# Performance work log

Hardware: AMD Instinct MI355X
Metric: run time of the kernel (lower is better)

## Reference

```python
import jax, jax.numpy as jnp
import numpy as np

D_MODEL = 1024
N_HEADS = 16
HEAD_DIM = D_MODEL // N_HEADS
ROPE_BASE = 10000.0


def setup_inputs() -> dict:
    key = jax.random.key(0)
    ks = jax.random.split(key, 5)
    B, S = 4, 2048
    bound_qkv = 1.0 / np.sqrt(D_MODEL)
    bound_out = 1.0 / np.sqrt(D_MODEL)
    return {
        "query": jax.random.normal(ks[0], (B, S, D_MODEL), dtype=jnp.float32),
        "W_qkv": jax.random.uniform(ks[1], (3 * D_MODEL, D_MODEL), jnp.float32, -bound_qkv, bound_qkv),
        "b_qkv": jax.random.uniform(ks[2], (3 * D_MODEL,), jnp.float32, -bound_qkv, bound_qkv),
        "W_out": jax.random.uniform(ks[3], (D_MODEL, D_MODEL), jnp.float32, -bound_out, bound_out),
        "b_out": jax.random.uniform(ks[4], (D_MODEL,), jnp.float32, -bound_out, bound_out),
    }


def _rope(x):
    # x: [B, H, S, Dh]; rotate-half RoPE, full rotational fraction
    S, Dh = x.shape[2], x.shape[3]
    half = Dh // 2
    inv_freq = 1.0 / (ROPE_BASE ** (jnp.arange(0, half, dtype=jnp.float32) * 2.0 / Dh))
    ang = jnp.arange(S, dtype=jnp.float32)[:, None] * inv_freq[None, :]  # [S, half]
    cos = jnp.concatenate([jnp.cos(ang), jnp.cos(ang)], axis=-1)  # [S, Dh]
    sin = jnp.concatenate([jnp.sin(ang), jnp.sin(ang)], axis=-1)
    x1, x2 = x[..., :half], x[..., half:]
    rot = jnp.concatenate([-x2, x1], axis=-1)
    return x * cos + rot * sin


def reference(query, W_qkv, b_qkv, W_out, b_out):
    B, S, _ = query.shape
    qkv = query @ W_qkv.T + b_qkv  # [B, S, 3*D]
    qkv = qkv.reshape(B, S, 3, N_HEADS, HEAD_DIM).transpose(2, 0, 3, 1, 4)  # [3, B, H, S, Dh]
    q, k, v = qkv[0], qkv[1], qkv[2]
    q = _rope(q)
    k = _rope(k)
    scale = 1.0 / np.sqrt(HEAD_DIM)
    scores = jnp.einsum("bhsd,bhtd->bhst", q, k) * scale  # [B, H, S, S]
    attn = jax.nn.softmax(scores, axis=-1)
    out = jnp.einsum("bhst,bhtd->bhsd", attn, v)  # [B, H, S, Dh]
    out = out.transpose(0, 2, 1, 3).reshape(B, S, D_MODEL)
    return out @ W_out.T + b_out
```

## Files before the change

kernel.cpp:

```cpp
#include <hip/hip_runtime.h>
#include <math.h>

#define D_MODEL 1024
#define N_HEADS 16
#define HEAD_DIM 64
#define BATCH 4
#define SEQ 2048
#define TOKENS (BATCH * SEQ)

typedef _Float16 f16;
typedef f16 f16x8_t __attribute__((ext_vector_type(8)));
typedef f16 f16x4_t __attribute__((ext_vector_type(4)));
typedef float f32x4_t __attribute__((ext_vector_type(4)));

#define QSCALE 0.18033688011112042f

#define KSW(row, g) ((g) ^ ((row) & 7))

__device__ __forceinline__ void stage16(const f16* g, f16* l) {
    __builtin_amdgcn_global_load_lds(
        (__attribute__((address_space(1))) void*)g,
        (__attribute__((address_space(3))) void*)l, 16, 0, 0);
}

#define N_X  (TOKENS * D_MODEL / 4)
#define N_WQ (3 * D_MODEL * D_MODEL / 4)
#define N_WO (D_MODEL * D_MODEL / 4)
#define N_CONV (N_X + N_WQ + N_WO)
__global__ void prep_kernel(const float* __restrict__ X,
                            const float* __restrict__ Wq,
                            const float* __restrict__ Wo,
                            f16* __restrict__ Xf, f16* __restrict__ Wqf,
                            f16* __restrict__ Wof,
                            float* __restrict__ cosT, float* __restrict__ sinT) {
    int i = blockIdx.x * blockDim.x + threadIdx.x;
    if (i >= N_CONV) {
        int idx = i - N_CONV;
        int s = idx >> 5;
        int ii = idx & 31;
        double t = (double)(2 * ii) / 64.0;
        double invf = pow(10000.0, -t);
        double ang = (double)s * invf;
        cosT[idx] = (float)cos(ang);
        sinT[idx] = (float)sin(ang);
        return;
    }
    const float* src;
    f16* dst;
    int j;
    if (i < N_X)             { src = X;  dst = Xf;  j = i; }
    else if (i < N_X + N_WQ) { src = Wq; dst = Wqf; j = i - N_X; }
    else                     { src = Wo; dst = Wof; j = i - N_X - N_WQ; }
    float4 x = ((const float4*)src)[j];
    f16x4_t h;
    h[0] = (f16)x.x; h[1] = (f16)x.y; h[2] = (f16)x.z; h[3] = (f16)x.w;
    ((f16x4_t*)dst)[j] = h;
}

__device__ __forceinline__ void gemm_mainloop(
    const f16* __restrict__ A, const f16* __restrict__ B,
    int n0, int c0, f16* As, f16* Bs, f32x4_t acc[4][4]) {
    const int tid = threadIdx.x;
    const int lane = tid & 63;
    const int wave = tid >> 6;
    const int m16 = lane & 15, quad = lane >> 4;
    const int wm = (wave & 1) * 64, wn = (wave >> 1) * 64;

    const int srow  = lane >> 3;
    const int sgran = (lane & 7) ^ srow;

#pragma unroll
    for (int i = 0; i < 4; i++)
#pragma unroll
        for (int j = 0; j < 4; j++) acc[i][j] = (f32x4_t){0.f, 0.f, 0.f, 0.f};

    f16* ldsA = As + (wave * 32) * 64;
    f16* ldsB = Bs + (wave * 32) * 64;
    const f16* ga = A + (size_t)(n0 + wave * 32 + srow) * D_MODEL + sgran * 8;
    const f16* gb = B + (size_t)(c0 + wave * 32 + srow) * D_MODEL + sgran * 8;

    for (int kt = 0; kt < 16; kt++) {
        const int ko = kt * 64;
        __syncthreads();
#pragma unroll
        for (int inst = 0; inst < 4; inst++) {
            stage16(ga + ko + (size_t)(inst * 8) * D_MODEL, ldsA + inst * 8 * 64);
            stage16(gb + ko + (size_t)(inst * 8) * D_MODEL, ldsB + inst * 8 * 64);
        }
        __syncthreads();
#pragma unroll
        for (int kk = 0; kk < 2; kk++) {
            f16x8_t a[4], b[4];
#pragma unroll
            for (int mt = 0; mt < 4; mt++) {
                const int row = wm + mt * 16 + m16;
                a[mt] = *(const f16x8_t*)&As[row * 64 + KSW(row, kk * 4 + quad) * 8];
            }
#pragma unroll
            for (int nt = 0; nt < 4; nt++) {
                const int row = wn + nt * 16 + m16;
                b[nt] = *(const f16x8_t*)&Bs[row * 64 + KSW(row, kk * 4 + quad) * 8];
            }
#pragma unroll
            for (int mt = 0; mt < 4; mt++)
#pragma unroll
                for (int nt = 0; nt < 4; nt++)
                    acc[mt][nt] = __builtin_amdgcn_mfma_f32_16x16x32_f16(
                        a[mt], b[nt], acc[mt][nt], 0, 0, 0);
        }
    }
}

__global__ __launch_bounds__(256)
void qkv_gemm_kernel(const f16* __restrict__ Xf, const f16* __restrict__ Wf,
                     const float* __restrict__ bias,
                     f16* __restrict__ Qb, f16* __restrict__ Kb,
                     f16* __restrict__ VbT,
                     const float* __restrict__ cosT, const float* __restrict__ sinT) {
    __shared__ f16 As[128 * 64];
    __shared__ f16 Bs[128 * 64];
    f32x4_t acc[4][4];
    const int n0 = blockIdx.y * 128;
    const int c0 = blockIdx.x * 128;
    gemm_mainloop(Xf, Wf, n0, c0, As, Bs, acc);

    const int lane = threadIdx.x & 63;
    const int wave = threadIdx.x >> 6;
    const int m16 = lane & 15, quad = lane >> 4;
    const int wm = (wave & 1) * 64, wn = (wave >> 1) * 64;

    const int w = c0 >> 10;
    const int hh = ((c0 + wn) & 1023) >> 6;
    const int b = n0 >> 11;

    float bias4[4];
#pragma unroll
    for (int nt = 0; nt < 4; nt++) bias4[nt] = bias[c0 + wn + nt * 16 + m16];

    if (w == 2) {
        f16* vbase = VbT + ((size_t)(b * N_HEADS + hh) * HEAD_DIM) * SEQ;
#pragma unroll
        for (int mt = 0; mt < 4; mt++) {
            const int sbl = (n0 + wm + (mt >> 1) * 32) & (SEQ - 1);
            const int sb  = sbl + quad * 8 + (mt & 1) * 4;
#pragma unroll
            for (int nt = 0; nt < 4; nt++) {
                const int dh = nt * 16 + m16;
                f16x4_t v4;
#pragma unroll
                for (int i = 0; i < 4; i++) v4[i] = (f16)(acc[mt][nt][i] + bias4[nt]);
                *(f16x4_t*)&vbase[(size_t)dh * SEQ + sb] = v4;
            }
        }
        return;
    }

    f16* dst = (w == 0) ? Qb : Kb;
#pragma unroll
    for (int mt = 0; mt < 4; mt++)
#pragma unroll
        for (int i = 0; i < 4; i++) {
            const int n = n0 + wm + mt * 16 + quad * 4 + i;
            const int s = n & (SEQ - 1);
            f16* drow = dst + ((size_t)(b * N_HEADS + hh) * SEQ + s) * HEAD_DIM;
            float vv[4];
#pragma unroll
            for (int nt = 0; nt < 4; nt++) vv[nt] = acc[mt][nt][i] + bias4[nt];
            const float cs0 = cosT[(s << 5) + m16];
            const float sn0 = sinT[(s << 5) + m16];
            const float cs1 = cosT[(s << 5) + 16 + m16];
            const float sn1 = sinT[(s << 5) + 16 + m16];
#pragma unroll
            for (int nt = 0; nt < 4; nt++) {
                const int dh = nt * 16 + m16;
                const float cs = (nt & 1) ? cs1 : cs0;
                const float sn = (nt & 1) ? sn1 : sn0;
                const float part = vv[nt ^ 2];
                float outv = (nt >= 2) ? fmaf(vv[nt], cs, part * sn)
                                       : fmaf(vv[nt], cs, -part * sn);
                if (w == 0) outv *= QSCALE;
                drow[dh] = (f16)outv;
            }
        }
}

__global__ __launch_bounds__(256)
void out_gemm_kernel(const f16* __restrict__ Of, const f16* __restrict__ Wf,
                     const float* __restrict__ bias, float* __restrict__ Cout) {
    __shared__ f16 As[128 * 64];
    __shared__ f16 Bs[128 * 64];
    f32x4_t acc[4][4];
    const int n0 = blockIdx.y * 128;
    const int c0 = blockIdx.x * 128;
    gemm_mainloop(Of, Wf, n0, c0, As, Bs, acc);

    const int lane = threadIdx.x & 63;
    const int wave = threadIdx.x >> 6;
    const int m16 = lane & 15, quad = lane >> 4;
    const int wm = (wave & 1) * 64, wn = (wave >> 1) * 64;

    float bias4[4];
#pragma unroll
    for (int nt = 0; nt < 4; nt++) bias4[nt] = bias[c0 + wn + nt * 16 + m16];

#pragma unroll
    for (int mt = 0; mt < 4; mt++)
#pragma unroll
        for (int i = 0; i < 4; i++) {
            const int n = n0 + wm + mt * 16 + quad * 4 + i;
            float* orow = Cout + (size_t)n * D_MODEL + c0 + wn;
#pragma unroll
            for (int nt = 0; nt < 4; nt++)
                orow[nt * 16 + m16] = acc[mt][nt][i] + bias4[nt];
        }
}

#define NT (SEQ / 64)
__global__ __launch_bounds__(256, 2)
void attn_kernel(const f16* __restrict__ Qb, const f16* __restrict__ Kb,
                 const f16* __restrict__ VbT, f16* __restrict__ Of) {
    __shared__ f16 Ks[2][64 * 64];
    __shared__ f16 Vs[2][64 * 64];

    const int tid  = threadIdx.x;
    const int lane = tid & 63;
    const int wave = tid >> 6;
    const int m16  = lane & 15;
    const int quad = lane >> 4;

    const int bh = blockIdx.x & 63;
    const int qt = blockIdx.x >> 6;
    const int s0 = qt * 256;

    const f16* Kbase  = Kb + (size_t)bh * SEQ * HEAD_DIM;
    const f16* VtBase = VbT + (size_t)bh * HEAD_DIM * SEQ;

    f16x8_t bq[4][2];
#pragma unroll
    for (int nq = 0; nq < 4; nq++) {
        const f16* qrow = Qb + ((size_t)bh * SEQ + s0 + wave * 64 + nq * 16 + m16)
                          * HEAD_DIM + quad * 8;
        bq[nq][0] = *(const f16x8_t*)(qrow);
        bq[nq][1] = *(const f16x8_t*)(qrow + 32);
    }

    f32x4_t Oc[4][4];
#pragma unroll
    for (int mt = 0; mt < 4; mt++)
#pragma unroll
        for (int nq = 0; nq < 4; nq++) Oc[mt][nq] = (f32x4_t){0.f, 0.f, 0.f, 0.f};
    float sumacc[4] = {0.f, 0.f, 0.f, 0.f};

    const int lrow0 = wave * 16 + (lane >> 3);
    const int lrow1 = lrow0 + 8;
    const int gK0 = lrow0 * HEAD_DIM + KSW(lrow0, lane & 7) * 8;
    const int gK1 = lrow1 * HEAD_DIM + KSW(lrow1, lane & 7) * 8;
    const int gV0 = lrow0 * SEQ + KSW(lrow0, lane & 7) * 8;
    const int gV1 = lrow1 * SEQ + KSW(lrow1, lane & 7) * 8;
    const int lO0 = (wave * 16) * 64;
    const int lO1 = (wave * 16 + 8) * 64;

    stage16(Kbase + gK0, &Ks[0][lO0]);
    stage16(Kbase + gK1, &Ks[0][lO1]);
    stage16(VtBase + gV0, &Vs[0][lO0]);
    stage16(VtBase + gV1, &Vs[0][lO1]);
    asm volatile("s_waitcnt vmcnt(0)" ::: "memory");
    __builtin_amdgcn_s_barrier();
    asm volatile("" ::: "memory");

    for (int kt = 0; kt < NT; kt++) {
        const int cur = kt & 1;

        if (kt + 1 < NT) {
            const f16* kg = Kbase + (size_t)(kt + 1) * 64 * HEAD_DIM;
            const f16* vg = VtBase + (kt + 1) * 64;
            f16* kd = &Ks[cur ^ 1][0];
            f16* vd = &Vs[cur ^ 1][0];
            stage16(kg + gK0, kd + lO0);
            stage16(kg + gK1, kd + lO1);
            stage16(vg + gV0, vd + lO0);
            stage16(vg + gV1, vd + lO1);
        }

        const f16* Kc = &Ks[cur][0];
        const f16* Vc = &Vs[cur][0];

        f32x4_t Sc[4][4];
#pragma unroll
        for (int nt = 0; nt < 4; nt++)
#pragma unroll
            for (int nq = 0; nq < 4; nq++) Sc[nt][nq] = (f32x4_t){0.f, 0.f, 0.f, 0.f};
#pragma unroll
        for (int kki = 0; kki < 2; kki++) {
#pragma unroll
            for (int nt = 0; nt < 4; nt++) {
                const int row = nt * 16 + m16;
                f16x8_t ak = *(const f16x8_t*)&Kc[row * 64 + KSW(row, kki * 4 + quad) * 8];
                __builtin_amdgcn_s_setprio(1);
#pragma unroll
                for (int nq = 0; nq < 4; nq++)
                    Sc[nt][nq] = __builtin_amdgcn_mfma_f32_16x16x32_f16(
                        ak, bq[nq][kki], Sc[nt][nq], 0, 0, 0);
                __builtin_amdgcn_s_setprio(0);
            }
        }

#pragma unroll
        for (int kki = 0; kki < 2; kki++) {
            f16x8_t bp[4];
#pragma unroll
            for (int nq = 0; nq < 4; nq++)
#pragma unroll
                for (int h = 0; h < 2; h++) {
                    const int nt = 2 * kki + h;
#pragma unroll
                    for (int i = 0; i < 4; i++) {
                        float p = __builtin_amdgcn_exp2f(Sc[nt][nq][i]);
                        sumacc[nq] += p;
                        bp[nq][h * 4 + i] = (f16)p;
                    }
                }
#pragma unroll
            for (int mt = 0; mt < 4; mt++) {
                const int d = mt * 16 + m16;
                f16x8_t av = *(const f16x8_t*)&Vc[d * 64 + KSW(d, kki * 4 + quad) * 8];
                __builtin_amdgcn_s_setprio(1);
#pragma unroll
                for (int nq = 0; nq < 4; nq++)
                    Oc[mt][nq] = __builtin_amdgcn_mfma_f32_16x16x32_f16(
                        av, bp[nq], Oc[mt][nq], 0, 0, 0);
                __builtin_amdgcn_s_setprio(0);
            }
        }

        asm volatile("s_waitcnt vmcnt(0)" ::: "memory");
        __builtin_amdgcn_s_barrier();
        asm volatile("" ::: "memory");
    }

    const int b = bh >> 4, h = bh & 15;
#pragma unroll
    for (int nq = 0; nq < 4; nq++) {
        float l = sumacc[nq];
        l += __shfl_xor(l, 16);
        l += __shfl_xor(l, 32);
        const float invl = 1.0f / l;
        const int s = s0 + wave * 64 + nq * 16 + m16;
        const size_t off = ((size_t)(b * SEQ + s)) * D_MODEL + h * HEAD_DIM;
#pragma unroll
        for (int mt = 0; mt < 4; mt++) {
            f16x4_t o4;
#pragma unroll
            for (int i = 0; i < 4; i++)
                o4[i] = (f16)(Oc[mt][nq][i] * invl);
            *(f16x4_t*)&Of[off + mt * 16 + quad * 4] = o4;
        }
    }
}

extern "C" void kernel_launch(void* const* d_in, const int* in_sizes, int n_in,
                              void* d_out, int out_size, void* d_ws, size_t ws_size,
                              hipStream_t stream) {
    const float* X    = (const float*)d_in[0];
    const float* Wqkv = (const float*)d_in[1];
    const float* bqkv = (const float*)d_in[2];
    const float* Wout = (const float*)d_in[3];
    const float* bout = (const float*)d_in[4];
    float* out = (float*)d_out;

    char* w8 = (char*)d_ws;
    const size_t MB = 1024 * 1024;
    f16* Xf  = (f16*)(w8);
    f16* Wqf = (f16*)(w8 + 16 * MB);
    f16* Wof = (f16*)(w8 + 22 * MB);
    f16* Qf  = (f16*)(w8 + 24 * MB);
    f16* Kf  = (f16*)(w8 + 40 * MB);
    f16* VfT = (f16*)(w8 + 56 * MB);
    f16* Of  = (f16*)(w8 + 72 * MB);
    float* cosT = (float*)(w8 + 88 * MB);
    float* sinT = cosT + SEQ * 32;

    prep_kernel<<<(N_CONV + SEQ * 32) / 256, 256, 0, stream>>>(
        X, Wqkv, Wout, Xf, Wqf, Wof, cosT, sinT);

    qkv_gemm_kernel<<<dim3(3 * D_MODEL / 128, TOKENS / 128), 256, 0, stream>>>(
        Xf, Wqf, bqkv, Qf, Kf, VfT, cosT, sinT);
    attn_kernel<<<64 * (SEQ / 256), 256, 0, stream>>>(Qf, Kf, VfT, Of);
    out_gemm_kernel<<<dim3(D_MODEL / 128, TOKENS / 128), 256, 0, stream>>>(
        Of, Wof, bout, out);
}
```

Before: 270.5 us.

## Double-buffer GEMM mainloop LDS staging with BK=32 and prefetch next tile

```diff
diff --git a/kernel.cpp b/kernel.cpp
--- a/kernel.cpp
+++ b/kernel.cpp
@@ -16,6 +16,7 @@
 #define QSCALE 0.18033688011112042f
 
 #define KSW(row, g) ((g) ^ ((row) & 7))
+#define GSW(row, g) ((g) ^ (((row) >> 1) & 3))
 
 __device__ __forceinline__ void stage16(const f16* g, f16* l) {
     __builtin_amdgcn_global_load_lds(
@@ -57,6 +58,10 @@
     ((f16x4_t*)dst)[j] = h;
 }
 
+#define GBK 32
+#define GNKT (D_MODEL / GBK)
+#define GBUF (128 * GBK)
+
 __device__ __forceinline__ void gemm_mainloop(
     const f16* __restrict__ A, const f16* __restrict__ B,
     int n0, int c0, f16* As, f16* Bs, f32x4_t acc[4][4]) {
@@ -66,48 +71,64 @@
     const int m16 = lane & 15, quad = lane >> 4;
     const int wm = (wave & 1) * 64, wn = (wave >> 1) * 64;
 
-    const int srow  = lane >> 3;
-    const int sgran = (lane & 7) ^ srow;
+    const int srow = lane >> 2;
+    const int sg   = (lane & 3) ^ ((lane >> 3) & 3);
 
 #pragma unroll
     for (int i = 0; i < 4; i++)
 #pragma unroll
         for (int j = 0; j < 4; j++) acc[i][j] = (f32x4_t){0.f, 0.f, 0.f, 0.f};
 
-    f16* ldsA = As + (wave * 32) * 64;
-    f16* ldsB = Bs + (wave * 32) * 64;
-    const f16* ga = A + (size_t)(n0 + wave * 32 + srow) * D_MODEL + sgran * 8;
-    const f16* gb = B + (size_t)(c0 + wave * 32 + srow) * D_MODEL + sgran * 8;
-
-    for (int kt = 0; kt < 16; kt++) {
-        const int ko = kt * 64;
-        __syncthreads();
-#pragma unroll
-        for (int inst = 0; inst < 4; inst++) {
-            stage16(ga + ko + (size_t)(inst * 8) * D_MODEL, ldsA + inst * 8 * 64);
-            stage16(gb + ko + (size_t)(inst * 8) * D_MODEL, ldsB + inst * 8 * 64);
-        }
-        __syncthreads();
-#pragma unroll
-        for (int kk = 0; kk < 2; kk++) {
-            f16x8_t a[4], b[4];
-#pragma unroll
-            for (int mt = 0; mt < 4; mt++) {
-                const int row = wm + mt * 16 + m16;
-                a[mt] = *(const f16x8_t*)&As[row * 64 + KSW(row, kk * 4 + quad) * 8];
-            }
-#pragma unroll
-            for (int nt = 0; nt < 4; nt++) {
-                const int row = wn + nt * 16 + m16;
-                b[nt] = *(const f16x8_t*)&Bs[row * 64 + KSW(row, kk * 4 + quad) * 8];
-            }
-#pragma unroll
-            for (int mt = 0; mt < 4; mt++)
-#pragma unroll
-                for (int nt = 0; nt < 4; nt++)
-                    acc[mt][nt] = __builtin_amdgcn_mfma_f32_16x16x32_f16(
-                        a[mt], b[nt], acc[mt][nt], 0, 0, 0);
-        }
+    const f16* ga = A + (size_t)(n0 + wave * 32 + srow) * D_MODEL + sg * 8;
+    const f16* gb = B + (size_t)(c0 + wave * 32 + srow) * D_MODEL + sg * 8;
+    f16* la = As + (wave * 32) * GBK;
+    f16* lb = Bs + (wave * 32) * GBK;
+
+    stage16(ga, la);
+    stage16(ga + (size_t)16 * D_MODEL, la + 16 * GBK);
+    stage16(gb, lb);
+    stage16(gb + (size_t)16 * D_MODEL, lb + 16 * GBK);
+    asm volatile("s_waitcnt vmcnt(0)" ::: "memory");
+    __builtin_amdgcn_s_barrier();
+    asm volatile("" ::: "memory");
+
+    for (int kt = 0; kt < GNKT; kt++) {
+        const int cur = kt & 1;
+
+        if (kt + 1 < GNKT) {
+            const int ko = (kt + 1) * GBK;
+            const int nb = (cur ^ 1) * GBUF;
+            stage16(ga + ko, la + nb);
+            stage16(ga + ko + (size_t)16 * D_MODEL, la + nb + 16 * GBK);
+            stage16(gb + ko, lb + nb);
+            stage16(gb + ko + (size_t)16 * D_MODEL, lb + nb + 16 * GBK);
+        }
+
+        const f16* Ac = As + cur * GBUF;
+        const f16* Bc = Bs + cur * GBUF;
+        f16x8_t a[4], b[4];
+#pragma unroll
+        for (int mt = 0; mt < 4; mt++) {
+            const int row = wm + mt * 16 + m16;
+            a[mt] = *(const f16x8_t*)&Ac[row * GBK + GSW(row, quad) * 8];
+        }
+#pragma unroll
+        for (int nt = 0; nt < 4; nt++) {
+            const int row = wn + nt * 16 + m16;
+            b[nt] = *(const f16x8_t*)&Bc[row * GBK + GSW(row, quad) * 8];
+        }
+        __builtin_amdgcn_s_setprio(1);
+#pragma unroll
+        for (int mt = 0; mt < 4; mt++)
+#pragma unroll
+            for (int nt = 0; nt < 4; nt++)
+                acc[mt][nt] = __builtin_amdgcn_mfma_f32_16x16x32_f16(
+                    a[mt], b[nt], acc[mt][nt], 0, 0, 0);
+        __builtin_amdgcn_s_setprio(0);
+
+        asm volatile("s_waitcnt vmcnt(0)" ::: "memory");
+        __builtin_amdgcn_s_barrier();
+        asm volatile("" ::: "memory");
     }
 }
 
@@ -117,8 +138,8 @@
                      f16* __restrict__ Qb, f16* __restrict__ Kb,
                      f16* __restrict__ VbT,
                      const float* __restrict__ cosT, const float* __restrict__ sinT) {
-    __shared__ f16 As[128 * 64];
-    __shared__ f16 Bs[128 * 64];
+    __shared__ f16 As[2 * GBUF];
+    __shared__ f16 Bs[2 * GBUF];
     f32x4_t acc[4][4];
     const int n0 = blockIdx.y * 128;
     const int c0 = blockIdx.x * 128;
@@ -187,8 +208,8 @@
 __global__ __launch_bounds__(256)
 void out_gemm_kernel(const f16* __restrict__ Of, const f16* __restrict__ Wf,
                      const float* __restrict__ bias, float* __restrict__ Cout) {
-    __shared__ f16 As[128 * 64];
-    __shared__ f16 Bs[128 * 64];
+    __shared__ f16 As[2 * GBUF];
+    __shared__ f16 Bs[2 * GBUF];
     f32x4_t acc[4][4];
     const int n0 = blockIdx.y * 128;
     const int c0 = blockIdx.x * 128;
```

Measured after the change: 285.3 us. 1.05x slower.
